# Kernel tuning notes

Hardware: AMD Instinct MI355X
Metric: run time of the kernel (lower is better)

Reference implementation:

```python
import jax, jax.numpy as jnp
import numpy as np

B, T, D_IN, H1, H2, K = 16, 1024, 384, 1024, 1024, 9


def _l2normalize(w, axis):
    # matches F.normalize(w, dim=axis): w / max(||w||_2, 1e-12)
    n = jnp.sqrt(jnp.sum(w * w, axis=axis, keepdims=True))
    return w / jnp.maximum(n, 1e-12)


def _mish(x):
    return x * jnp.tanh(jax.nn.softplus(x))


def setup_inputs() -> dict:
    key = jax.random.key(0)
    ks = jax.random.split(key, 11)
    f32 = jnp.float32
    return {
        "input": jax.random.normal(ks[0], (B, T, D_IN), f32),
        "d_w": jax.random.normal(ks[1], (B, H1, 1, K), f32),
        "d_g": jax.random.normal(ks[2], (B, H1), f32),
        "d_b": jax.random.normal(ks[3], (B, H1), f32),
        "p_w": jax.random.normal(ks[4], (B, H1, H2, 1), f32),
        "p_g": jax.random.normal(ks[5], (B, H1), f32),
        "p_b": jax.random.normal(ks[6], (B, H2), f32),
        "w1_w": jax.random.normal(ks[7], (H1, D_IN), f32) * 0.05,
        "w1_b": jax.random.normal(ks[8], (H1,), f32) * 0.05,
        "w2_w": jax.random.normal(ks[9], (D_IN, H2), f32) * 0.05,
        "w2_b": jax.random.normal(ks[10], (D_IN,), f32) * 0.05,
    }


def reference(input, d_w, d_g, d_b, p_w, p_g, p_b, w1_w, w1_b, w2_w, w2_b):
    residual = input
    # w_1: 1x1 conv == per-position linear, then Mish (dropout = identity in eval)
    h = _mish(jnp.einsum('btc,hc->bth', input, w1_w) + w1_b)   # [B,T,H1]
    x = jnp.transpose(h, (0, 2, 1))                            # [B,H1,T]
    k = d_w.shape[-1]
    pad = (k - 1) // 2
    t = x.shape[-1]
    xp = jnp.pad(x, ((0, 0), (0, 0), (pad, pad)))              # [B,H1,T+2p]
    idx = jnp.arange(t)[:, None] + jnp.arange(k)[None, :]      # [T,K]
    xu = xp[:, :, idx]                                         # [B,H1,T,K] (unfold)
    # weight-normalized dynamic depthwise conv weights
    dwn = _l2normalize(d_w, axis=1) * d_g[:, :, None, None]    # [B,H1,1,K]
    # torch.einsum('bctk,bcwk->bct') with d_w expanded along w(=T): w is summed,
    # and every w-slice is identical, so the dot product picks up a factor of T.
    y = jnp.einsum('bctk,bck->bct', xu, dwn[:, :, 0, :]) * t   # [B,H1,T]
    y = y + d_b[:, :, None]
    # weight-normalized dynamic pointwise mix
    pwn = _l2normalize(p_w, axis=1) * p_g[:, :, None, None]    # [B,H1,H2,1]
    z = jnp.einsum('bct,bco->bot', y, pwn[..., 0])             # [B,H2,T]
    z = z + p_b[:, :, None]
    # w_2: 1x1 conv back to d_in, residual add
    out2 = jnp.einsum('bot,do->btd', z, w2_w) + w2_b           # [B,T,D_IN]
    return out2 + residual
```

## Files before the change

kernel.cpp:

```cpp
#include <hip/hip_runtime.h>

#define BCNT 16
#define TT 1024
#define DIN 384
#define H1 1024
#define H2 1024
#define KW 9

typedef __attribute__((ext_vector_type(8))) short bhalf8;
typedef __attribute__((ext_vector_type(4))) float f32x4;

typedef const __attribute__((address_space(1))) void* gas_ptr;
typedef __attribute__((address_space(3))) void* lds_ptr;

__device__ __forceinline__ float bf2f(unsigned short u) {
    return __uint_as_float(((unsigned int)u) << 16);
}
__device__ __forceinline__ unsigned short f2bf(float f) {
    unsigned int u = __float_as_uint(f);
    unsigned int r = (u + 0x7FFFu + ((u >> 16) & 1u)) >> 16;
    return (unsigned short)r;
}
__device__ __forceinline__ float mish_f(float x) {
    if (x > 20.f) return x;
    float u = __expf(x);
    float n = u * u + 2.f * u;
    return x * n / (n + 2.f);
}


__global__ __launch_bounds__(256) void k_cvt3z(
    const float* __restrict__ s0, unsigned short* __restrict__ d0, int n0,
    const float* __restrict__ s1, unsigned short* __restrict__ d1, int n1,
    const float* __restrict__ s2, unsigned short* __restrict__ d2, int n2,
    float* __restrict__ zb, int n3) {
    int i = blockIdx.x * 256 + threadIdx.x;
    const float* s; unsigned short* d; int j = i;
    if (i < n0) { s = s0; d = d0; }
    else if ((j = i - n0) < n1) { s = s1; d = d1; }
    else if ((j = i - n0 - n1) < n2) { s = s2; d = d2; }
    else if ((j = i - n0 - n1 - n2) < n3) {
        ((float4*)zb)[j] = make_float4(0.f, 0.f, 0.f, 0.f);
        return;
    } else return;
    float4 v = ((const float4*)s)[j];
    ushort4 o;
    o.x = f2bf(v.x); o.y = f2bf(v.y); o.z = f2bf(v.z); o.w = f2bf(v.w);
    ((ushort4*)d)[j] = o;
}

__global__ void k_norm_dwn(const float* __restrict__ d_w, const float* __restrict__ d_g,
                           float* __restrict__ dwn_s) {
    int idx = blockIdx.x;
    int b = idx / KW, k = idx % KW;
    float s = 0.f;
    for (int c = threadIdx.x; c < H1; c += 256) {
        float v = d_w[((size_t)b * H1 + c) * KW + k];
        s += v * v;
    }
    __shared__ float red[256];
    __shared__ float nsh;
    red[threadIdx.x] = s; __syncthreads();
    for (int st = 128; st > 0; st >>= 1) {
        if (threadIdx.x < st) red[threadIdx.x] += red[threadIdx.x + st];
        __syncthreads();
    }
    if (threadIdx.x == 0) nsh = fmaxf(sqrtf(red[0]), 1e-12f);
    __syncthreads();
    float n = nsh;
    for (int c = threadIdx.x; c < H1; c += 256) {
        size_t o = ((size_t)b * H1 + c) * KW + k;
        dwn_s[o] = d_w[o] / n * d_g[b * H1 + c] * (float)TT;
    }
}

__global__ __launch_bounds__(256) void k_tpw3(const float* __restrict__ p_w,
                                              const float* __restrict__ p_g,
                                              unsigned short* __restrict__ pwTu,
                                              float* __restrict__ sumsq) {
    __shared__ float tile[32][132];
    __shared__ float sred[8][32][4];
    __shared__ float pg[32];
    const int tid = threadIdx.x;
    const int tx = tid & 31, ty = tid >> 5;
    const int c0 = blockIdx.x * 32, o0 = blockIdx.y * 128, b = blockIdx.z;
    if (tid < 32) pg[tid] = p_g[(size_t)b * H1 + c0 + tid];
    const float4* pw4 = (const float4*)p_w;
    float s0 = 0.f, s1 = 0.f, s2 = 0.f, s3 = 0.f;
#pragma unroll
    for (int j = 0; j < 4; j++) {
        int cl = ty + j * 8;
        float4 v = pw4[(size_t)(b * H1 + c0 + cl) * (H2 / 4) + (o0 / 4) + tx];
        *(float4*)&tile[cl][tx * 4] = v;
        s0 += v.x * v.x; s1 += v.y * v.y; s2 += v.z * v.z; s3 += v.w * v.w;
    }
    sred[ty][tx][0] = s0; sred[ty][tx][1] = s1;
    sred[ty][tx][2] = s2; sred[ty][tx][3] = s3;
    __syncthreads();
    if (tid < 128) {
        int txo = tid >> 2, q = tid & 3;
        float t = 0.f;
#pragma unroll
        for (int r = 0; r < 8; r++) t += sred[r][txo][q];
        atomicAdd(&sumsq[(size_t)b * H2 + o0 + txo * 4 + q], t);
    }
    const int ol = tid >> 1, half = (tid & 1) * 16;
    unsigned short outv[16];
#pragma unroll
    for (int i = 0; i < 16; i++)
        outv[i] = f2bf(tile[half + i][ol] * pg[half + i]);
    unsigned short* dst = &pwTu[((size_t)b * H2 + o0 + ol) * H1 + c0 + half];
    *(bhalf8*)dst = *(const bhalf8*)&outv[0];
    *(bhalf8*)&dst[8] = *(const bhalf8*)&outv[8];
}

__global__ __launch_bounds__(256) void k_conv4(const unsigned short* __restrict__ h,
                                               const float* __restrict__ dwn_s,
                                               const float* __restrict__ d_b,
                                               unsigned short* __restrict__ y) {
    const int tid = threadIdx.x;
    const int c = tid * 4;
    const int t0 = blockIdx.x * 16;
    const int b = blockIdx.z;
    const ushort4* hb = (const ushort4*)(h + (size_t)b * TT * H1);
    ushort4* yb = (ushort4*)(y + (size_t)b * TT * H1);
    float kk[KW][4], db[4];
#pragma unroll
    for (int q = 0; q < 4; q++) {
        db[q] = d_b[b * H1 + c + q];
#pragma unroll
        for (int i = 0; i < KW; i++)
            kk[i][q] = dwn_s[((size_t)b * H1 + c + q) * KW + i];
    }
    float w[KW][4];
#pragma unroll
    for (int i = 0; i < 8; i++) {
        int t = t0 - 4 + i;
        if (t >= 0) {
            ushort4 v = hb[(size_t)t * (H1 / 4) + tid];
            w[i][0] = bf2f(v.x); w[i][1] = bf2f(v.y);
            w[i][2] = bf2f(v.z); w[i][3] = bf2f(v.w);
        } else { w[i][0] = w[i][1] = w[i][2] = w[i][3] = 0.f; }
    }
#pragma unroll
    for (int j = 0; j < 16; j++) {
        const int t = t0 + j, tl = t + 4;
        if (tl < TT) {
            ushort4 v = hb[(size_t)tl * (H1 / 4) + tid];
            w[8][0] = bf2f(v.x); w[8][1] = bf2f(v.y);
            w[8][2] = bf2f(v.z); w[8][3] = bf2f(v.w);
        } else { w[8][0] = w[8][1] = w[8][2] = w[8][3] = 0.f; }
        float a0 = db[0], a1 = db[1], a2 = db[2], a3 = db[3];
#pragma unroll
        for (int i = 0; i < KW; i++) {
            a0 += kk[i][0] * w[i][0]; a1 += kk[i][1] * w[i][1];
            a2 += kk[i][2] * w[i][2]; a3 += kk[i][3] * w[i][3];
        }
        ushort4 o;
        o.x = f2bf(a0); o.y = f2bf(a1); o.z = f2bf(a2); o.w = f2bf(a3);
        yb[(size_t)t * (H1 / 4) + tid] = o;
#pragma unroll
        for (int i = 0; i < 8; i++) {
            w[i][0] = w[i + 1][0]; w[i][1] = w[i + 1][1];
            w[i][2] = w[i + 1][2]; w[i][3] = w[i + 1][3];
        }
    }
}

template <int MODE, int GS>
__global__ __launch_bounds__(512, 2) void gemm_dp(
    const unsigned short* __restrict__ A, const unsigned short* __restrict__ Bm,
    unsigned short* __restrict__ Cp, int Kdim, int lda, int ldb, int ldc,
    long sA, long sB, long sC,
    const float* __restrict__ bias, int biasStride,
    const float* __restrict__ sumsq) {
    __shared__ __attribute__((aligned(16))) unsigned short As[3][128 * 64];
    __shared__ __attribute__((aligned(16))) unsigned short Bs[3][128 * 64];

    const int tid = threadIdx.x;
    const int lane = tid & 63, wv = tid >> 6;
    const int wr = wv >> 2, wc = wv & 3;

    int bx, by, bz;
    {
        int l = blockIdx.x;
        int xcd = l & 7, s = l >> 3;
        if constexpr (GS == 0) { bz = 0; bx = xcd * 8 + (s & 7); by = s >> 3; }
        else { bz = xcd * 2 + (s >> 4); int u = s & 15; bx = u & 3; by = u >> 2; }
    }
    const int bm = bx * 256, bn = by * 256;
    const unsigned short* Ab = A + (size_t)sA * bz;
    const unsigned short* Bb = Bm + (size_t)sB * bz;

    const int rSl = lane >> 3;
    const int gSl = (lane & 7) ^ (rSl & 7);
    const int mOf = 2 * rSl + (gSl >> 2);
    const int kOf = (gSl & 3) * 8;

    const int l16 = lane & 15, quad = lane >> 4;
    const int Rb = l16 >> 1;
    const int gsw = ((l16 & 1) * 4 + quad) ^ (Rb & 7);
    const int aoff = (wr * 64 + Rb) * 64 + gsw * 8;
    const int boff = (wc * 32 + Rb) * 64 + gsw * 8;

    f32x4 acc[8][4];
#pragma unroll
    for (int i = 0; i < 8; i++)
#pragma unroll
        for (int j = 0; j < 4; j++)
#pragma unroll
            for (int r = 0; r < 4; r++) acc[i][j][r] = 0.f;

    auto STAGE_A = [&](int kt) {
        const int slot = kt % 3;
        const int kofs = kt * 32 + kOf;
#pragma unroll
        for (int i = 0; i < 2; i++) {
            const int ch = wv + i * 8;
            const unsigned short* ga = Ab + (size_t)(bm + ch * 16 + mOf) * lda + kofs;
            __builtin_amdgcn_global_load_lds((gas_ptr)ga, (lds_ptr)&As[slot][ch * 512], 16, 0, 0);
        }
    };
    auto STAGE_B = [&](int kt) {
        const int slot = kt % 3;
        const int kofs = kt * 32 + kOf;
#pragma unroll
        for (int i = 0; i < 2; i++) {
            const int ch = wv + i * 8;
            const unsigned short* gb = Bb + (size_t)(bn + ch * 16 + mOf) * ldb + kofs;
            __builtin_amdgcn_global_load_lds((gas_ptr)gb, (lds_ptr)&Bs[slot][ch * 512], 16, 0, 0);
        }
    };

    const int nkt = Kdim / 32;
    STAGE_A(0); STAGE_B(0);
    STAGE_A(1); STAGE_B(1);
    asm volatile("s_waitcnt vmcnt(4)" ::: "memory");
    __builtin_amdgcn_s_barrier();

    for (int kt = 0; kt < nkt; ++kt) {
        const unsigned short* Asl = &As[kt % 3][0];
        const unsigned short* Bsl = &Bs[kt % 3][0];
        const bool pf = (kt + 2 < nkt);

        bhalf8 bfv[4], afv[4];
        bfv[0] = *(const bhalf8*)&Bsl[boff];
        bfv[1] = *(const bhalf8*)&Bsl[boff + 512];
        bfv[2] = *(const bhalf8*)&Bsl[boff + 1024];
        bfv[3] = *(const bhalf8*)&Bsl[boff + 1536];
        afv[0] = *(const bhalf8*)&Asl[aoff];
        afv[1] = *(const bhalf8*)&Asl[aoff + 512];
        afv[2] = *(const bhalf8*)&Asl[aoff + 1024];
        afv[3] = *(const bhalf8*)&Asl[aoff + 1536];
        if (pf) STAGE_A(kt + 2);
        __builtin_amdgcn_sched_barrier(0);
        __builtin_amdgcn_s_barrier();
        asm volatile("s_waitcnt lgkmcnt(0)" ::: "memory");
        __builtin_amdgcn_sched_barrier(0);
        __builtin_amdgcn_s_setprio(1);
#pragma unroll
        for (int mi = 0; mi < 4; mi++)
#pragma unroll
            for (int ni = 0; ni < 4; ni++)
                acc[mi][ni] = __builtin_amdgcn_mfma_f32_16x16x32_bf16(
                    afv[mi], bfv[ni], acc[mi][ni], 0, 0, 0);
        __builtin_amdgcn_s_setprio(0);
        __builtin_amdgcn_s_barrier();

        bhalf8 afw[4];
        afw[0] = *(const bhalf8*)&Asl[aoff + 4 * 512];
        afw[1] = *(const bhalf8*)&Asl[aoff + 5 * 512];
        afw[2] = *(const bhalf8*)&Asl[aoff + 6 * 512];
        afw[3] = *(const bhalf8*)&Asl[aoff + 7 * 512];
        if (pf) STAGE_B(kt + 2);
        __builtin_amdgcn_sched_barrier(0);
        __builtin_amdgcn_s_barrier();
        asm volatile("s_waitcnt lgkmcnt(0)" ::: "memory");
        __builtin_amdgcn_sched_barrier(0);
        __builtin_amdgcn_s_setprio(1);
#pragma unroll
        for (int mi = 0; mi < 4; mi++)
#pragma unroll
            for (int ni = 0; ni < 4; ni++)
                acc[4 + mi][ni] = __builtin_amdgcn_mfma_f32_16x16x32_bf16(
                    afw[mi], bfv[ni], acc[4 + mi][ni], 0, 0, 0);
        __builtin_amdgcn_s_setprio(0);
        if (pf) asm volatile("s_waitcnt vmcnt(4)" ::: "memory");
        else    asm volatile("s_waitcnt vmcnt(0)" ::: "memory");
        __builtin_amdgcn_s_barrier();
    }

#pragma unroll
    for (int mi = 0; mi < 8; mi++)
#pragma unroll
        for (int ni = 0; ni < 4; ni++)
#pragma unroll
            for (int r = 0; r < 4; r++) {
                int gm = bm + wr * 128 + mi * 16 + quad * 4 + r;
                int gn = bn + wc * 64 + ni * 16 + l16;
                float v = acc[mi][ni][r];
                size_t cidx = (size_t)sC * bz + (size_t)gm * ldc + gn;
                if constexpr (MODE == 0) {
                    v = mish_f(v + bias[gn]);
                    Cp[cidx] = f2bf(v);
                } else {
                    size_t si = (size_t)bz * biasStride + gn;
                    float rr = rsqrtf(fmaxf(sumsq[si], 1e-24f));
                    v = v * rr + bias[si];
                    Cp[cidx] = f2bf(v);
                }
            }
}

template <int MODE, int SWIZ, int TN>
__global__ __launch_bounds__(256, 4) void gemm_nt(
    const unsigned short* __restrict__ A, const unsigned short* __restrict__ Bm,
    void* __restrict__ Cp, int Kdim, int lda, int ldb, int ldc,
    long sA, long sB, long sC,
    const float* __restrict__ bias, int biasStride,
    const float* __restrict__ sumsq,
    const unsigned short* __restrict__ residbf) {
    constexpr int WN = TN / 32;
    __shared__ __attribute__((aligned(16))) unsigned short Al[128 * 64];
    __shared__ __attribute__((aligned(16))) unsigned short Bl[TN * 64];

    const int tid = threadIdx.x;
    const int lane = tid & 63, wv = tid >> 6;

    int bx, by, bz;
    if constexpr (SWIZ) {
        int l = blockIdx.x;
        int xcd = l & 7, s = l >> 3;
        bz = xcd * 2 + (s >> 6);
        int u = s & 63;
        bx = u & 7; by = u >> 3;
    } else {
        bx = blockIdx.x; by = blockIdx.y; bz = blockIdx.z;
    }
    const int bm = bx * 128, bn = by * TN;

    const unsigned short* Ab = A + (size_t)sA * bz;
    const unsigned short* Bb = Bm + (size_t)sB * bz;

    const int rS = lane >> 3;
    const int cS = ((lane & 7) ^ (rS & 7)) * 8;

    const int wm = (wv >> 1) * 64, wn = (wv & 1) * (TN / 2);
    const int l16 = lane & 15, quad = lane >> 4;
    const int fx = l16 & 7;

    f32x4 acc[4][WN];
#pragma unroll
    for (int i = 0; i < 4; i++)
#pragma unroll
        for (int j = 0; j < WN; j++)
#pragma unroll
            for (int r = 0; r < 4; r++) acc[i][j][r] = 0.f;

    const int ktiles = Kdim / 64;
    for (int kt = 0; kt < ktiles; ++kt) {
        const int kofs = kt * 64 + cS;
#pragma unroll
        for (int i = 0; i < 4; i++) {
            const int ch = i * 4 + wv;
            const unsigned short* ga = Ab + (size_t)(bm + ch * 8 + rS) * lda + kofs;
            __builtin_amdgcn_global_load_lds((gas_ptr)ga, (lds_ptr)&Al[ch * 512], 16, 0, 0);
        }
#pragma unroll
        for (int i = 0; i < TN / 32; i++) {
            const int ch = i * 4 + wv;
            const unsigned short* gb = Bb + (size_t)(bn + ch * 8 + rS) * ldb + kofs;
            __builtin_amdgcn_global_load_lds((gas_ptr)gb, (lds_ptr)&Bl[ch * 512], 16, 0, 0);
        }
        __syncthreads();

#pragma unroll
        for (int kk = 0; kk < 2; kk++) {
            const int cg = ((kk * 4 + quad) ^ fx) * 8;
            bhalf8 af[4], bf[WN];
#pragma unroll
            for (int mi = 0; mi < 4; mi++)
                af[mi] = *(const bhalf8*)&Al[(wm + mi * 16 + l16) * 64 + cg];
#pragma unroll
            for (int ni = 0; ni < WN; ni++)
                bf[ni] = *(const bhalf8*)&Bl[(wn + ni * 16 + l16) * 64 + cg];
#pragma unroll
            for (int mi = 0; mi < 4; mi++)
#pragma unroll
                for (int ni = 0; ni < WN; ni++)
                    acc[mi][ni] = __builtin_amdgcn_mfma_f32_16x16x32_bf16(af[mi], bf[ni],
                                                                         acc[mi][ni], 0, 0, 0);
        }
        __syncthreads();
    }

#pragma unroll
    for (int mi = 0; mi < 4; mi++)
#pragma unroll
        for (int ni = 0; ni < WN; ni++)
#pragma unroll
            for (int r = 0; r < 4; r++) {
                int gm = bm + wm + mi * 16 + quad * 4 + r;
                int gn = bn + wn + ni * 16 + l16;
                float v = acc[mi][ni][r];
                size_t cidx = (size_t)sC * bz + (size_t)gm * ldc + gn;
                if constexpr (MODE == 0) {
                    v = mish_f(v + bias[gn]);
                    ((unsigned short*)Cp)[cidx] = f2bf(v);
                } else if constexpr (MODE == 1) {
                    size_t si = (size_t)bz * biasStride + gn;
                    float rr = rsqrtf(fmaxf(sumsq[si], 1e-24f));
                    v = v * rr + bias[si];
                    ((unsigned short*)Cp)[cidx] = f2bf(v);
                } else {
                    v += bias[gn] + bf2f(residbf[cidx]);
                    ((float*)Cp)[cidx] = v;
                }
            }
}


extern "C" void kernel_launch(void* const* d_in, const int* in_sizes, int n_in,
                              void* d_out, int out_size, void* d_ws, size_t ws_size,
                              hipStream_t stream) {
    const float* input = (const float*)d_in[0];
    const float* d_w   = (const float*)d_in[1];
    const float* d_g   = (const float*)d_in[2];
    const float* d_b   = (const float*)d_in[3];
    const float* p_w   = (const float*)d_in[4];
    const float* p_g   = (const float*)d_in[5];
    const float* p_b   = (const float*)d_in[6];
    const float* w1_w  = (const float*)d_in[7];
    const float* w1_b  = (const float*)d_in[8];
    const float* w2_w  = (const float*)d_in[9];
    const float* w2_b  = (const float*)d_in[10];
    float* out = (float*)d_out;

    char* ws = (char*)d_ws;
    size_t off = 0;
    auto alloc = [&](size_t bytes) {
        char* p = ws + off;
        off += (bytes + 255) & ~(size_t)255;
        return p;
    };
    float* dwn_s         = (float*)alloc((size_t)BCNT * H1 * KW * 4);
    float* sumsq         = (float*)alloc((size_t)BCNT * H2 * 4);
    unsigned short* inbf = (unsigned short*)alloc((size_t)BCNT * TT * DIN * 2);
    unsigned short* w1bf = (unsigned short*)alloc((size_t)H1 * DIN * 2);
    unsigned short* w2bf = (unsigned short*)alloc((size_t)DIN * H2 * 2);
    unsigned short* h    = (unsigned short*)alloc((size_t)BCNT * TT * H1 * 2);
    unsigned short* y    = (unsigned short*)alloc((size_t)BCNT * TT * H1 * 2);
    unsigned short* pwTu = (unsigned short*)alloc((size_t)BCNT * H2 * H1 * 2);
    unsigned short* zt   = (unsigned short*)alloc((size_t)BCNT * TT * H2 * 2);

    const int n4_in = BCNT * TT * DIN / 4, n4_w1 = H1 * DIN / 4, n4_w2 = DIN * H2 / 4;
    const int n4_z = BCNT * H2 / 4;
    k_cvt3z<<<(n4_in + n4_w1 + n4_w2 + n4_z + 255) / 256, 256, 0, stream>>>(
        input, inbf, n4_in, w1_w, w1bf, n4_w1, w2_w, w2bf, n4_w2, sumsq, n4_z);

    k_norm_dwn<<<BCNT * KW, 256, 0, stream>>>(d_w, d_g, dwn_s);
    k_tpw3<<<dim3(H1 / 32, H2 / 128, BCNT), 256, 0, stream>>>(p_w, p_g, pwTu, sumsq);

    gemm_dp<0, 0><<<256, 512, 0, stream>>>(
        inbf, w1bf, h, DIN, DIN, DIN, H1, 0, 0, 0, w1_b, 0, nullptr);

    k_conv4<<<dim3(TT / 16, 1, BCNT), 256, 0, stream>>>(h, dwn_s, d_b, y);

    gemm_dp<1, 1><<<256, 512, 0, stream>>>(
        y, pwTu, zt, H1, H1, H1, H2, (long)TT * H1, (long)H2 * H1, (long)TT * H2,
        p_b, H2, sumsq);

    gemm_nt<2, 0, 64><<<dim3(BCNT * TT / 128, DIN / 64, 1), 256, 0, stream>>>(
        zt, w2bf, out, H2, H2, H2, DIN, 0, 0, 0, w2_b, 0, nullptr, inbf);
}
```

Before: 269.6 us.

## Software-pipeline LDS fragment loads in big GEMM, route first GEMM to gemm_nt

Rewrites the large batched GEMM main loop so the next k-tile's A/B fragments are loaded from LDS while the second half of the current tile's MFMAs run. It uses double-buffered register fragments and partial lgkmcnt waits. A and B global-to-LDS staging are merged into one call per iteration, which cuts the barriers per k-step from four to two. The first GEMM (input x w1) now uses the existing gemm_nt kernel with 128-wide tiles instead of the 256x256 gemm_dp. This raises register pressure, and it assumes nkt is even and that the lgkmcnt counts match the issued loads.

New measurement: 264.4 us. About the same (-2.0%).

```diff
diff --git a/kernel.cpp b/kernel.cpp
--- a/kernel.cpp
+++ b/kernel.cpp
@@ -167,8 +167,61 @@
     }
 }
 
+#define LH_STEP(KT, BFC, AFC, BFN, AFN)                                        \
+  {                                                                            \
+    const unsigned short* Asl = &As[(KT) % 3][0];                              \
+    bhalf8 afw0 = *(const bhalf8*)&Asl[aoff + 4 * 512];                        \
+    bhalf8 afw1 = *(const bhalf8*)&Asl[aoff + 5 * 512];                        \
+    bhalf8 afw2 = *(const bhalf8*)&Asl[aoff + 6 * 512];                        \
+    bhalf8 afw3 = *(const bhalf8*)&Asl[aoff + 7 * 512];                        \
+    if ((KT) + 2 < nkt) STAGE((KT) + 2);                                       \
+    asm volatile("s_waitcnt lgkmcnt(4)" ::: "memory");                         \
+    __builtin_amdgcn_sched_barrier(0);                                         \
+    __builtin_amdgcn_s_setprio(1);                                             \
+    _Pragma("unroll") for (int mi = 0; mi < 4; mi++)                           \
+      _Pragma("unroll") for (int ni = 0; ni < 4; ni++)                         \
+        acc[mi][ni] = __builtin_amdgcn_mfma_f32_16x16x32_bf16(                 \
+            AFC[mi], BFC[ni], acc[mi][ni], 0, 0, 0);                           \
+    __builtin_amdgcn_s_setprio(0);                                             \
+    if ((KT) + 2 < nkt) asm volatile("s_waitcnt vmcnt(4)" ::: "memory");       \
+    else                asm volatile("s_waitcnt vmcnt(0)" ::: "memory");       \
+    __builtin_amdgcn_s_barrier();                                              \
+    __builtin_amdgcn_sched_barrier(0);                                         \
+    if ((KT) + 1 < nkt) {                                                      \
+      const unsigned short* Asn = &As[((KT) + 1) % 3][0];                      \
+      const unsigned short* Bsn = &Bs[((KT) + 1) % 3][0];                      \
+      BFN[0] = *(const bhalf8*)&Bsn[boff];                                     \
+      BFN[1] = *(const bhalf8*)&Bsn[boff + 512];                               \
+      BFN[2] = *(const bhalf8*)&Bsn[boff + 1024];                              \
+      BFN[3] = *(const bhalf8*)&Bsn[boff + 1536];                              \
+      AFN[0] = *(const bhalf8*)&Asn[aoff];                                     \
+      AFN[1] = *(const bhalf8*)&Asn[aoff + 512];                               \
+      AFN[2] = *(const bhalf8*)&Asn[aoff + 1024];                              \
+      AFN[3] = *(const bhalf8*)&Asn[aoff + 1536];                              \
+      asm volatile("s_waitcnt lgkmcnt(8)" ::: "memory");                       \
+    } else {                                                                   \
+      asm volatile("s_waitcnt lgkmcnt(0)" ::: "memory");                       \
+    }                                                                          \
+    __builtin_amdgcn_sched_barrier(0);                                         \
+    __builtin_amdgcn_s_setprio(1);                                             \
+    _Pragma("unroll") for (int ni = 0; ni < 4; ni++)                           \
+      acc[4][ni] = __builtin_amdgcn_mfma_f32_16x16x32_bf16(afw0, BFC[ni],      \
+                                                           acc[4][ni], 0, 0, 0);\
+    _Pragma("unroll") for (int ni = 0; ni < 4; ni++)                           \
+      acc[5][ni] = __builtin_amdgcn_mfma_f32_16x16x32_bf16(afw1, BFC[ni],      \
+                                                           acc[5][ni], 0, 0, 0);\
+    _Pragma("unroll") for (int ni = 0; ni < 4; ni++)                           \
+      acc[6][ni] = __builtin_amdgcn_mfma_f32_16x16x32_bf16(afw2, BFC[ni],      \
+                                                           acc[6][ni], 0, 0, 0);\
+    _Pragma("unroll") for (int ni = 0; ni < 4; ni++)                           \
+      acc[7][ni] = __builtin_amdgcn_mfma_f32_16x16x32_bf16(afw3, BFC[ni],      \
+                                                           acc[7][ni], 0, 0, 0);\
+    __builtin_amdgcn_s_setprio(0);                                             \
+    __builtin_amdgcn_s_barrier();                                              \
+  }
+
 template <int MODE, int GS>
-__global__ __launch_bounds__(512, 2) void gemm_dp(
+__global__ __launch_bounds__(512, 2) void gemm_lh(
     const unsigned short* __restrict__ A, const unsigned short* __restrict__ Bm,
     unsigned short* __restrict__ Cp, int Kdim, int lda, int ldb, int ldc,
     long sA, long sB, long sC,
@@ -211,7 +264,7 @@
 #pragma unroll
             for (int r = 0; r < 4; r++) acc[i][j][r] = 0.f;
 
-    auto STAGE_A = [&](int kt) {
+    auto STAGE = [&](int kt) {
         const int slot = kt % 3;
         const int kofs = kt * 32 + kOf;
 #pragma unroll
@@ -219,75 +272,34 @@
             const int ch = wv + i * 8;
             const unsigned short* ga = Ab + (size_t)(bm + ch * 16 + mOf) * lda + kofs;
             __builtin_amdgcn_global_load_lds((gas_ptr)ga, (lds_ptr)&As[slot][ch * 512], 16, 0, 0);
-        }
-    };
-    auto STAGE_B = [&](int kt) {
-        const int slot = kt % 3;
-        const int kofs = kt * 32 + kOf;
-#pragma unroll
-        for (int i = 0; i < 2; i++) {
-            const int ch = wv + i * 8;
             const unsigned short* gb = Bb + (size_t)(bn + ch * 16 + mOf) * ldb + kofs;
             __builtin_amdgcn_global_load_lds((gas_ptr)gb, (lds_ptr)&Bs[slot][ch * 512], 16, 0, 0);
         }
     };
 
     const int nkt = Kdim / 32;
-    STAGE_A(0); STAGE_B(0);
-    STAGE_A(1); STAGE_B(1);
+    STAGE(0); STAGE(1);
     asm volatile("s_waitcnt vmcnt(4)" ::: "memory");
     __builtin_amdgcn_s_barrier();
-
-    for (int kt = 0; kt < nkt; ++kt) {
-        const unsigned short* Asl = &As[kt % 3][0];
-        const unsigned short* Bsl = &Bs[kt % 3][0];
-        const bool pf = (kt + 2 < nkt);
-
-        bhalf8 bfv[4], afv[4];
-        bfv[0] = *(const bhalf8*)&Bsl[boff];
-        bfv[1] = *(const bhalf8*)&Bsl[boff + 512];
-        bfv[2] = *(const bhalf8*)&Bsl[boff + 1024];
-        bfv[3] = *(const bhalf8*)&Bsl[boff + 1536];
-        afv[0] = *(const bhalf8*)&Asl[aoff];
-        afv[1] = *(const bhalf8*)&Asl[aoff + 512];
-        afv[2] = *(const bhalf8*)&Asl[aoff + 1024];
-        afv[3] = *(const bhalf8*)&Asl[aoff + 1536];
-        if (pf) STAGE_A(kt + 2);
-        __builtin_amdgcn_sched_barrier(0);
-        __builtin_amdgcn_s_barrier();
-        asm volatile("s_waitcnt lgkmcnt(0)" ::: "memory");
-        __builtin_amdgcn_sched_barrier(0);
-        __builtin_amdgcn_s_setprio(1);
-#pragma unroll
-        for (int mi = 0; mi < 4; mi++)
-#pragma unroll
-            for (int ni = 0; ni < 4; ni++)
-                acc[mi][ni] = __builtin_amdgcn_mfma_f32_16x16x32_bf16(
-                    afv[mi], bfv[ni], acc[mi][ni], 0, 0, 0);
-        __builtin_amdgcn_s_setprio(0);
-        __builtin_amdgcn_s_barrier();
-
-        bhalf8 afw[4];
-        afw[0] = *(const bhalf8*)&Asl[aoff + 4 * 512];
-        afw[1] = *(const bhalf8*)&Asl[aoff + 5 * 512];
-        afw[2] = *(const bhalf8*)&Asl[aoff + 6 * 512];
-        afw[3] = *(const bhalf8*)&Asl[aoff + 7 * 512];
-        if (pf) STAGE_B(kt + 2);
-        __builtin_amdgcn_sched_barrier(0);
-        __builtin_amdgcn_s_barrier();
-        asm volatile("s_waitcnt lgkmcnt(0)" ::: "memory");
-        __builtin_amdgcn_sched_barrier(0);
-        __builtin_amdgcn_s_setprio(1);
-#pragma unroll
-        for (int mi = 0; mi < 4; mi++)
-#pragma unroll
-            for (int ni = 0; ni < 4; ni++)
-                acc[4 + mi][ni] = __builtin_amdgcn_mfma_f32_16x16x32_bf16(
-                    afw[mi], bfv[ni], acc[4 + mi][ni], 0, 0, 0);
-        __builtin_amdgcn_s_setprio(0);
-        if (pf) asm volatile("s_waitcnt vmcnt(4)" ::: "memory");
-        else    asm volatile("s_waitcnt vmcnt(0)" ::: "memory");
-        __builtin_amdgcn_s_barrier();
+    __builtin_amdgcn_sched_barrier(0);
+
+    bhalf8 bfE[4], afE[4], bfO[4], afO[4];
+    {
+        const unsigned short* As0 = &As[0][0];
+        const unsigned short* Bs0 = &Bs[0][0];
+        bfE[0] = *(const bhalf8*)&Bs0[boff];
+        bfE[1] = *(const bhalf8*)&Bs0[boff + 512];
+        bfE[2] = *(const bhalf8*)&Bs0[boff + 1024];
+        bfE[3] = *(const bhalf8*)&Bs0[boff + 1536];
+        afE[0] = *(const bhalf8*)&As0[aoff];
+        afE[1] = *(const bhalf8*)&As0[aoff + 512];
+        afE[2] = *(const bhalf8*)&As0[aoff + 1024];
+        afE[3] = *(const bhalf8*)&As0[aoff + 1536];
+    }
+
+    for (int kt = 0; kt < nkt; kt += 2) {
+        LH_STEP(kt, bfE, afE, bfO, afO);
+        LH_STEP(kt + 1, bfO, afO, bfE, afE);
     }
 
 #pragma unroll
@@ -461,12 +473,12 @@
     k_norm_dwn<<<BCNT * KW, 256, 0, stream>>>(d_w, d_g, dwn_s);
     k_tpw3<<<dim3(H1 / 32, H2 / 128, BCNT), 256, 0, stream>>>(p_w, p_g, pwTu, sumsq);
 
-    gemm_dp<0, 0><<<256, 512, 0, stream>>>(
-        inbf, w1bf, h, DIN, DIN, DIN, H1, 0, 0, 0, w1_b, 0, nullptr);
+    gemm_nt<0, 0, 128><<<dim3(BCNT * TT / 128, H1 / 128, 1), 256, 0, stream>>>(
+        inbf, w1bf, h, DIN, DIN, DIN, H1, 0, 0, 0, w1_b, 0, nullptr, nullptr);
 
     k_conv4<<<dim3(TT / 16, 1, BCNT), 256, 0, stream>>>(h, dwn_s, d_b, y);
 
-    gemm_dp<1, 1><<<256, 512, 0, stream>>>(
+    gemm_lh<1, 1><<<256, 512, 0, stream>>>(
         y, pwTu, zt, H1, H1, H1, H2, (long)TT * H1, (long)H2 * H1, (long)TT * H2,
         p_b, H2, sumsq);
 
```
